# Kernel tuning notes

Measured on AMD Instinct MI355X. Metric: run time of the kernel, lower is better.

## Reference

```python
import jax, jax.numpy as jnp
import numpy as np

N, L, S, D, H = 4, 8192, 8192, 256, 8
DH = D // H  # 32
EPS_ATTN = 1e-6
EPS_LN = 1e-5


def setup_inputs() -> dict:
    key = jax.random.key(0)
    ks = jax.random.split(key, 8)
    w = lambda k, sh: jax.random.normal(k, sh, jnp.float32) * 0.02
    return {
        "x": jax.random.normal(ks[0], (N, L, D), jnp.float32),
        "source": jax.random.normal(ks[1], (N, S, D), jnp.float32),
        "Wq": w(ks[2], (D, D)),
        "Wk": w(ks[3], (D, D)),
        "Wv": w(ks[4], (D, D)),
        "Wm": w(ks[5], (D, D)),
        "W1": w(ks[6], (2 * D, 2 * D)),
        "W2": w(ks[7], (2 * D, D)),
        "g1": jnp.ones((D,), jnp.float32),
        "b1": jnp.zeros((D,), jnp.float32),
        "g2": jnp.ones((D,), jnp.float32),
        "b2": jnp.zeros((D,), jnp.float32),
    }


def _layernorm(x, g, b):
    m = jnp.mean(x, axis=-1, keepdims=True)
    v = jnp.var(x, axis=-1, keepdims=True)
    return (x - m) * jax.lax.rsqrt(v + EPS_LN) * g + b


def reference(x, source, Wq, Wk, Wv, Wm, W1, W2, g1, b1, g2, b2):
    bs = x.shape[0]
    # QKV projections (bias=False), split heads -> [N, L/S, H, DH]
    q = (x @ Wq).reshape(bs, -1, H, DH)
    k = (source @ Wk).reshape(bs, -1, H, DH)
    v = (source @ Wv).reshape(bs, -1, H, DH)
    # elu+1 feature map (linear attention, LoFTR-style)
    Q = jax.nn.elu(q) + 1.0
    K = jax.nn.elu(k) + 1.0
    v_len = v.shape[1]
    vals = v / v_len
    KV = jnp.einsum("nshd,nshv->nhdv", K, vals)  # [N, H, DH, DH]
    Z = 1.0 / (jnp.einsum("nlhd,nhd->nlh", Q, K.sum(axis=1)) + EPS_ATTN)
    msg = jnp.einsum("nlhd,nhdv,nlh->nlhv", Q, KV, Z) * v_len  # [N, L, H, DH]
    # merge heads + LN
    msg = msg.reshape(bs, -1, H * DH) @ Wm
    msg = _layernorm(msg, g1, b1)
    # concat-MLP with LeakyReLU(0.1)
    h = jnp.concatenate([x, msg], axis=2) @ W1
    h = jnp.where(h >= 0, h, 0.1 * h)
    msg = h @ W2
    msg = _layernorm(msg, g2, b2)
    return x + msg
```

## Files before the change

### kernel.cpp

```cpp
#include <hip/hip_runtime.h>

typedef __bf16 bf16;
typedef __bf16 bf16x4 __attribute__((ext_vector_type(4)));
typedef __bf16 bf16x8 __attribute__((ext_vector_type(8)));
typedef float f32x4 __attribute__((ext_vector_type(4)));

__device__ __forceinline__ float apply_epi(float v, int epi) {
  if (epi == 1) return v > 0.f ? v + 1.f : __expf(v);
  if (epi == 2) return v >= 0.f ? v : 0.1f * v;
  return v;
}

__device__ __forceinline__ void g2l16(const bf16* gp, bf16* lp) {
  __builtin_amdgcn_global_load_lds(
      (const __attribute__((address_space(1))) void*)gp,
      (__attribute__((address_space(3))) void*)lp, 16, 0, 0);
}

__global__ void detect_kernel(const unsigned* g1raw, int* flag) {
  if (threadIdx.x == 0 && blockIdx.x == 0)
    *flag = (g1raw[0] == 0x3F800000u) ? 1 : 0;
}

struct TransArgs {
  const void* src[6];
  bf16* dst[6];
  int R[6], C[6], t0[6];
};

__global__ __launch_bounds__(256) void prep_kernel(
    const void* __restrict__ xin, const void* __restrict__ sin,
    bf16* __restrict__ bx, bf16* __restrict__ bs,
    TransArgs ta, const int* flagp) {
  const bool f32 = (*flagp != 0);
  if (blockIdx.x < 8192) {
    const void* s;
    bf16* d;
    size_t i;
    if (blockIdx.x < 4096) {
      s = xin; d = bx; i = (size_t)blockIdx.x * 2048 + threadIdx.x * 8;
    } else {
      s = sin; d = bs; i = (size_t)(blockIdx.x - 4096) * 2048 + threadIdx.x * 8;
    }
    if (f32) {
      f32x4 lo = *(const f32x4*)((const float*)s + i);
      f32x4 hi = *(const f32x4*)((const float*)s + i + 4);
      bf16x8 t;
      t[0] = (bf16)lo[0]; t[1] = (bf16)lo[1]; t[2] = (bf16)lo[2]; t[3] = (bf16)lo[3];
      t[4] = (bf16)hi[0]; t[5] = (bf16)hi[1]; t[6] = (bf16)hi[2]; t[7] = (bf16)hi[3];
      *(bf16x8*)(d + i) = t;
    } else {
      *(bf16x8*)(d + i) = *(const bf16x8*)((const bf16*)s + i);
    }
    return;
  }
  __shared__ bf16 tile[32][33];
  int bid = blockIdx.x - 8192;
  int si = 0;
#pragma unroll
  for (int i = 1; i < 6; ++i)
    if (bid >= ta.t0[i]) si = i;
  const void* srcv = ta.src[si];
  bf16* dst = ta.dst[si];
  int R = ta.R[si], Cc = ta.C[si];
  int lt = bid - ta.t0[si];
  int tpr = Cc >> 5;
  int tr = lt / tpr, tc = lt % tpr;
  int tx = threadIdx.x & 31, ty0 = threadIdx.x >> 5;
#pragma unroll
  for (int i = 0; i < 4; ++i) {
    int ty = ty0 + i * 8;
    size_t idx = (size_t)(tr * 32 + ty) * Cc + tc * 32 + tx;
    tile[ty][tx] = f32 ? (bf16)((const float*)srcv)[idx] : ((const bf16*)srcv)[idx];
  }
  __syncthreads();
#pragma unroll
  for (int i = 0; i < 4; ++i) {
    int ty = ty0 + i * 8;
    dst[(size_t)(tc * 32 + ty) * R + tr * 32 + tx] = tile[tx][ty];
  }
}

#define TM 256
#define TN 256
#define TK 64

__device__ __forceinline__ void stage_tile(
    const bf16* __restrict__ Ab, int ldA, int m0, int kcol,
    const bf16* __restrict__ Bt, int Kk, int n0, int kk,
    bf16* As, bf16* Bs, int tid) {
#pragma unroll
  for (int it = 0; it < 4; ++it) {
    int id = it * 512 + tid;
    int rr = id >> 3, pp = id & 7, gg = pp ^ (rr & 7);
    g2l16(Ab + (size_t)(m0 + rr) * ldA + kcol + gg * 8, As + id * 8);
  }
#pragma unroll
  for (int it = 0; it < 4; ++it) {
    int id = it * 512 + tid;
    int rr = id >> 3, pp = id & 7, gg = pp ^ (rr & 7);
    g2l16(Bt + (size_t)(n0 + rr) * Kk + kk + gg * 8, Bs + id * 8);
  }
}

__global__ __launch_bounds__(512, 2) void gemm256(
    const bf16* __restrict__ A, const bf16* __restrict__ A2, int ldA,
    const bf16* __restrict__ Bt, bf16* __restrict__ C, int Nn, int Kk, int epi,
    bf16* __restrict__ C2, int epi2, int split, int gridM) {
  __shared__ bf16 As[2][TM * TK];
  __shared__ bf16 Bs[2][TN * TK];
  const int tid = threadIdx.x;

  const int nwg = gridDim.x;
  const int cpx = nwg >> 3;
  const int swz = (blockIdx.x & 7) * cpx + (blockIdx.x >> 3);
  const int mb = swz % gridM, nb = swz / gridM;
  const int m0 = mb * TM, n0 = nb * TN;

  const int wave = tid >> 6, lane = tid & 63;
  const int wm = (wave >> 2) * 128, wn = (wave & 3) * 64;
  const int q = lane >> 4, mr = lane & 15;

  f32x4 acc[8][4];
#pragma unroll
  for (int i = 0; i < 8; ++i)
#pragma unroll
    for (int j = 0; j < 4; ++j) acc[i][j] = (f32x4){0.f, 0.f, 0.f, 0.f};

  const int kTiles = Kk / TK;

  stage_tile(A, ldA, m0, 0, Bt, Kk, n0, 0, As[0], Bs[0], tid);

  for (int kt = 0; kt < kTiles; ++kt) {
    const int nxt = kt + 1;
    if (nxt < kTiles) {
      int kk = nxt * TK;
      const bf16* Ab = A;
      int kcol = kk;
      if (A2 && kk >= 256) { Ab = A2; kcol = kk - 256; }
      stage_tile(Ab, ldA, m0, kcol, Bt, Kk, n0, kk, As[nxt & 1], Bs[nxt & 1], tid);
      asm volatile("s_waitcnt vmcnt(8)\n\ts_barrier" ::: "memory");
    } else {
      asm volatile("s_waitcnt vmcnt(0)\n\ts_barrier" ::: "memory");
    }
    const bf16* Asb = As[kt & 1];
    const bf16* Bsb = Bs[kt & 1];
#pragma unroll
    for (int ks = 0; ks < 2; ++ks) {
      bf16x8 af[8], bfv[4];
#pragma unroll
      for (int mi = 0; mi < 8; ++mi) {
        int rrow = wm + mi * 16 + mr;
        af[mi] = *(const bf16x8*)&Asb[rrow * TK + ((ks * 4 + q) ^ (rrow & 7)) * 8];
      }
#pragma unroll
      for (int ni = 0; ni < 4; ++ni) {
        int rrow = wn + ni * 16 + mr;
        bfv[ni] = *(const bf16x8*)&Bsb[rrow * TK + ((ks * 4 + q) ^ (rrow & 7)) * 8];
      }
#pragma unroll
      for (int mi = 0; mi < 8; ++mi)
#pragma unroll
        for (int ni = 0; ni < 4; ++ni)
          acc[mi][ni] = __builtin_amdgcn_mfma_f32_16x16x32_bf16(af[mi], bfv[ni], acc[mi][ni], 0, 0, 0);
    }
    asm volatile("s_waitcnt lgkmcnt(0)\n\ts_barrier" ::: "memory");
  }

  bf16* Cw = C;
  int nbase = n0, ep = epi;
  if (C2 && n0 >= split) { Cw = C2; nbase = n0 - split; ep = epi2; }
#pragma unroll
  for (int mi = 0; mi < 8; ++mi)
#pragma unroll
    for (int ni = 0; ni < 4; ++ni)
#pragma unroll
      for (int r4 = 0; r4 < 4; ++r4) {
        int row = m0 + wm + mi * 16 + q * 4 + r4;
        int cn = nbase + wn + ni * 16 + mr;
        float v = apply_epi(acc[mi][ni][r4], ep);
        Cw[(size_t)row * Nn + cn] = (bf16)v;
      }
}

#define KVCH 256
__global__ __launch_bounds__(256) void kv_kernel(
    const bf16* __restrict__ Kf, const bf16* __restrict__ V,
    float* __restrict__ partial, float* __restrict__ pk) {
  __shared__ bf16 Ks[KVCH][32];
  __shared__ bf16 Vs[KVCH][32];
  const int cb = blockIdx.x, h = blockIdx.y, n = blockIdx.z;
  const int tid = threadIdx.x;
  const int wave = tid >> 6, lane = tid & 63;
  const int d0 = (lane & 7) * 4, dv0 = (lane >> 3) * 4;
  const int s0 = cb * KVCH;
#pragma unroll
  for (int rd = 0; rd < 4; ++rd) {
    int rr = rd * 64 + (tid >> 2), pp = tid & 3;
    size_t g = ((size_t)(n * 8192 + s0 + rr)) * 256 + h * 32 + pp * 8;
    *(bf16x8*)&Ks[rr][pp * 8] = *(const bf16x8*)(Kf + g);
    *(bf16x8*)&Vs[rr][pp * 8] = *(const bf16x8*)(V + g);
  }
  __syncthreads();
  float acc[4][4] = {};
  float ks4[4] = {};
#pragma unroll 4
  for (int si = 0; si < 64; ++si) {
    int s = wave * 64 + si;
    bf16x4 k4 = *(const bf16x4*)&Ks[s][d0];
    bf16x4 v4 = *(const bf16x4*)&Vs[s][dv0];
    float kf[4] = {(float)k4[0], (float)k4[1], (float)k4[2], (float)k4[3]};
    float vf[4] = {(float)v4[0], (float)v4[1], (float)v4[2], (float)v4[3]};
#pragma unroll
    for (int vi = 0; vi < 4; ++vi)
#pragma unroll
      for (int di = 0; di < 4; ++di) acc[vi][di] = fmaf(vf[vi], kf[di], acc[vi][di]);
#pragma unroll
    for (int di = 0; di < 4; ++di) ks4[di] += kf[di];
  }
  __syncthreads();
  float* red = (float*)&Ks[0][0];
  float* ksr = (float*)&Vs[0][0];
#pragma unroll
  for (int vi = 0; vi < 4; ++vi)
#pragma unroll
    for (int di = 0; di < 4; ++di)
      red[wave * 1024 + (dv0 + vi) * 32 + d0 + di] = acc[vi][di];
  if (dv0 == 0) {
#pragma unroll
    for (int di = 0; di < 4; ++di) ksr[wave * 32 + d0 + di] = ks4[di];
  }
  __syncthreads();
  const size_t slot = (size_t)(n * 8 + h) * 32 + cb;
  f32x4 s4 = {0.f, 0.f, 0.f, 0.f};
#pragma unroll
  for (int w = 0; w < 4; ++w) s4 += *(const f32x4*)&red[w * 1024 + tid * 4];
  *(f32x4*)&partial[slot * 1024 + tid * 4] = s4;
  if (tid < 32) {
    float ss = 0.f;
#pragma unroll
    for (int w = 0; w < 4; ++w) ss += ksr[w * 32 + tid];
    pk[slot * 32 + tid] = ss;
  }
}

__global__ __launch_bounds__(256) void kv_reduce(
    const float* __restrict__ partial, const float* __restrict__ pk,
    float* __restrict__ kv_acc, float* __restrict__ ksum) {
  const int b = blockIdx.x;
  const int t = threadIdx.x;
  f32x4 s4 = {0.f, 0.f, 0.f, 0.f};
  for (int c = 0; c < 32; ++c)
    s4 += *(const f32x4*)&partial[((size_t)b * 32 + c) * 1024 + t * 4];
  *(f32x4*)&kv_acc[(size_t)b * 1024 + t * 4] = s4;
  if (t < 32) {
    float ss = 0.f;
    for (int c = 0; c < 32; ++c) ss += pk[((size_t)b * 32 + c) * 32 + t];
    ksum[(size_t)b * 32 + t] = ss;
  }
}

__global__ __launch_bounds__(256) void msg_kernel(
    const bf16* __restrict__ Q, const float* __restrict__ kv_acc,
    const float* __restrict__ ksum, bf16* __restrict__ msg) {
  __shared__ bf16 kvt[8][32][32];
  __shared__ float ksl[8][32];
  __shared__ float zl[8][128];
  int tid = threadIdx.x;
  int row0 = blockIdx.x * 128;
  int n = row0 >> 13;
  const float* kvb = kv_acc + (size_t)n * 8192;
  for (int i = tid; i < 8192; i += 256) ((bf16*)kvt)[i] = (bf16)kvb[i];
  ((float*)ksl)[tid] = ksum[(size_t)n * 256 + tid];
  __syncthreads();
  int r = tid & 127, hg = tid >> 7;
  const bf16* qrow = Q + (size_t)(row0 + r) * 256;
#pragma unroll
  for (int hh = 0; hh < 4; ++hh) {
    int h = hg * 4 + hh;
    float dot = 0.f;
#pragma unroll
    for (int d = 0; d < 32; ++d) dot = fmaf((float)qrow[h * 32 + d], ksl[h][d], dot);
    zl[h][r] = 1.f / (dot + 1e-6f);
  }
  __syncthreads();
  int wave = tid >> 6, lane = tid & 63, q = lane >> 4, mr = lane & 15;
  f32x4 zero = {0.f, 0.f, 0.f, 0.f};
  for (int h = 0; h < 8; ++h) {
    bf16x8 b0 = *(const bf16x8*)&kvt[h][mr][q * 8];
    bf16x8 b1 = *(const bf16x8*)&kvt[h][16 + mr][q * 8];
#pragma unroll
    for (int mi = 0; mi < 2; ++mi) {
      int arow = wave * 32 + mi * 16 + mr;
      bf16x8 a = *(const bf16x8*)(Q + (size_t)(row0 + arow) * 256 + h * 32 + q * 8);
      f32x4 c0 = __builtin_amdgcn_mfma_f32_16x16x32_bf16(a, b0, zero, 0, 0, 0);
      f32x4 c1 = __builtin_amdgcn_mfma_f32_16x16x32_bf16(a, b1, zero, 0, 0, 0);
#pragma unroll
      for (int r4 = 0; r4 < 4; ++r4) {
        int orow = wave * 32 + mi * 16 + q * 4 + r4;
        float z = zl[h][orow];
        size_t ob = (size_t)(row0 + orow) * 256 + h * 32;
        msg[ob + mr] = (bf16)(c0[r4] * z);
        msg[ob + 16 + mr] = (bf16)(c1[r4] * z);
      }
    }
  }
}

__global__ __launch_bounds__(256) void ln_kernel(
    const bf16* __restrict__ in, const void* __restrict__ g, const void* __restrict__ b,
    const void* __restrict__ resid, void* __restrict__ outp,
    const int* flagp, int ioDual) {
  const bool gbF32 = (*flagp != 0);
  const bool ioF32 = ioDual && gbF32;
  int wave = threadIdx.x >> 6, lane = threadIdx.x & 63;
  size_t row = (size_t)blockIdx.x * 4 + wave;
  int c = lane * 4;
  bf16x4 v = *(const bf16x4*)(in + row * 256 + c);
  float x0 = (float)v[0], x1 = (float)v[1], x2 = (float)v[2], x3 = (float)v[3];
  float s = x0 + x1 + x2 + x3;
  float sq = x0 * x0 + x1 * x1 + x2 * x2 + x3 * x3;
#pragma unroll
  for (int o = 32; o > 0; o >>= 1) {
    s += __shfl_xor(s, o);
    sq += __shfl_xor(sq, o);
  }
  float mean = s * (1.f / 256.f);
  float var = sq * (1.f / 256.f) - mean * mean;
  float rstd = rsqrtf(var + 1e-5f);
  float g0, g1v, g2v, g3, b0, b1v, b2v, b3;
  if (gbF32) {
    f32x4 gv = *(const f32x4*)((const float*)g + c);
    f32x4 bv = *(const f32x4*)((const float*)b + c);
    g0 = gv[0]; g1v = gv[1]; g2v = gv[2]; g3 = gv[3];
    b0 = bv[0]; b1v = bv[1]; b2v = bv[2]; b3 = bv[3];
  } else {
    bf16x4 gv = *(const bf16x4*)((const bf16*)g + c);
    bf16x4 bv = *(const bf16x4*)((const bf16*)b + c);
    g0 = (float)gv[0]; g1v = (float)gv[1]; g2v = (float)gv[2]; g3 = (float)gv[3];
    b0 = (float)bv[0]; b1v = (float)bv[1]; b2v = (float)bv[2]; b3 = (float)bv[3];
  }
  float y0 = (x0 - mean) * rstd * g0 + b0;
  float y1 = (x1 - mean) * rstd * g1v + b1v;
  float y2 = (x2 - mean) * rstd * g2v + b2v;
  float y3 = (x3 - mean) * rstd * g3 + b3;
  if (resid) {
    if (ioF32) {
      f32x4 rv = *(const f32x4*)((const float*)resid + row * 256 + c);
      y0 += rv[0]; y1 += rv[1]; y2 += rv[2]; y3 += rv[3];
    } else {
      bf16x4 rv = *(const bf16x4*)((const bf16*)resid + row * 256 + c);
      y0 += (float)rv[0]; y1 += (float)rv[1]; y2 += (float)rv[2]; y3 += (float)rv[3];
    }
  }
  if (ioF32) {
    f32x4 o4 = {y0, y1, y2, y3};
    *(f32x4*)((float*)outp + row * 256 + c) = o4;
  } else {
    bf16x4 o4;
    o4[0] = (bf16)y0; o4[1] = (bf16)y1; o4[2] = (bf16)y2; o4[3] = (bf16)y3;
    *(bf16x4*)((bf16*)outp + row * 256 + c) = o4;
  }
}

extern "C" void kernel_launch(void* const* d_in, const int* in_sizes, int n_in,
                              void* d_out, int out_size, void* d_ws, size_t ws_size,
                              hipStream_t stream) {
  const void* x   = d_in[0];
  const void* src = d_in[1];
  const void* Wq  = d_in[2];
  const void* Wk  = d_in[3];
  const void* Wv  = d_in[4];
  const void* Wm  = d_in[5];
  const void* W1  = d_in[6];
  const void* W2  = d_in[7];
  const void* g1  = d_in[8];
  const void* b1  = d_in[9];
  const void* g2  = d_in[10];
  const void* b2  = d_in[11];

  char* ws = (char*)d_ws;
  bf16* bufA = (bf16*)(ws);
  bf16* bufB = (bf16*)(ws + ((size_t)16 << 20));
  bf16* bufC = (bf16*)(ws + ((size_t)32 << 20));
  bf16* WqT  = (bf16*)(ws + ((size_t)48 << 20));
  bf16* WkvT = WqT + 65536;
  bf16* WmT  = WkvT + 131072;
  bf16* W1T  = WmT + 65536;
  bf16* W2T  = W1T + 262144;
  float* kv_acc = (float*)(ws + ((size_t)50 << 20));
  float* ksum = kv_acc + 32768;
  int* flagp = (int*)(ws + ((size_t)50 << 20) + 160 * 1024);
  float* partial = (float*)(ws + ((size_t)51 << 20));
  float* pk = (float*)(ws + ((size_t)55 << 20));
  bf16* bufX = (bf16*)d_out;
  bf16* bufS = bufX + 8388608;

  detect_kernel<<<dim3(1), dim3(64), 0, stream>>>((const unsigned*)g1, flagp);

  TransArgs ta;
  ta.src[0] = Wq; ta.src[1] = Wk; ta.src[2] = Wv; ta.src[3] = Wm; ta.src[4] = W1; ta.src[5] = W2;
  ta.dst[0] = WqT; ta.dst[1] = WkvT; ta.dst[2] = WkvT + 65536; ta.dst[3] = WmT; ta.dst[4] = W1T; ta.dst[5] = W2T;
  ta.R[0] = 256; ta.R[1] = 256; ta.R[2] = 256; ta.R[3] = 256; ta.R[4] = 512; ta.R[5] = 512;
  ta.C[0] = 256; ta.C[1] = 256; ta.C[2] = 256; ta.C[3] = 256; ta.C[4] = 512; ta.C[5] = 256;
  ta.t0[0] = 0; ta.t0[1] = 64; ta.t0[2] = 128; ta.t0[3] = 192; ta.t0[4] = 256; ta.t0[5] = 512;
  prep_kernel<<<dim3(8832), dim3(256), 0, stream>>>(x, src, bufX, bufS, ta, flagp);

  gemm256<<<dim3(128), dim3(512), 0, stream>>>(bufX, nullptr, 256, WqT, bufA, 256, 256, 1,
                                               nullptr, 0, 0, 128);
  gemm256<<<dim3(256), dim3(512), 0, stream>>>(bufS, nullptr, 256, WkvT, bufB, 256, 256, 1,
                                               bufC, 0, 256, 128);

  kv_kernel<<<dim3(32, 8, 4), dim3(256), 0, stream>>>(bufB, bufC, partial, pk);
  kv_reduce<<<dim3(32), dim3(256), 0, stream>>>(partial, pk, kv_acc, ksum);

  msg_kernel<<<dim3(256), dim3(256), 0, stream>>>(bufA, kv_acc, ksum, bufB);

  gemm256<<<dim3(128), dim3(512), 0, stream>>>(bufB, nullptr, 256, WmT, bufA, 256, 256, 0,
                                               nullptr, 0, 0, 128);

  ln_kernel<<<dim3(8192), dim3(256), 0, stream>>>(bufA, g1, b1, nullptr, bufC, flagp, 0);

  gemm256<<<dim3(256), dim3(512), 0, stream>>>(bufX, bufC, 256, W1T, bufA, 512, 512, 2,
                                               nullptr, 0, 0, 128);

  gemm256<<<dim3(128), dim3(512), 0, stream>>>(bufA, nullptr, 512, W2T, bufC, 256, 512, 0,
                                               nullptr, 0, 0, 128);

  ln_kernel<<<dim3(8192), dim3(256), 0, stream>>>(bufC, g2, b2, x, d_out, flagp, 1);
}
```

Before: 293.4 us.

## Restructure gemm256 main loop into phased half-tile staging interleaved with MFMA

The GEMM K-loop is rebuilt so that each 64-wide K tile is split into A and B halves of 128 rows. Global-to-LDS loads for upcoming halves are issued between sub-blocks of MFMA work, with fine-grained barriers and vmcnt waits, and s_setprio is raised around the MFMA clusters. The goal is to overlap memory staging with matrix math and to raise MFMA issue priority over other waves. The cost is many more barriers per tile and a more intricate schedule that assumes an even number of K tiles.

```diff
diff --git a/kernel.cpp b/kernel.cpp
--- a/kernel.cpp
+++ b/kernel.cpp
@@ -85,30 +85,11 @@
 #define TN 256
 #define TK 64
 
-__device__ __forceinline__ void stage_tile(
-    const bf16* __restrict__ Ab, int ldA, int m0, int kcol,
-    const bf16* __restrict__ Bt, int Kk, int n0, int kk,
-    bf16* As, bf16* Bs, int tid) {
-#pragma unroll
-  for (int it = 0; it < 4; ++it) {
-    int id = it * 512 + tid;
-    int rr = id >> 3, pp = id & 7, gg = pp ^ (rr & 7);
-    g2l16(Ab + (size_t)(m0 + rr) * ldA + kcol + gg * 8, As + id * 8);
-  }
-#pragma unroll
-  for (int it = 0; it < 4; ++it) {
-    int id = it * 512 + tid;
-    int rr = id >> 3, pp = id & 7, gg = pp ^ (rr & 7);
-    g2l16(Bt + (size_t)(n0 + rr) * Kk + kk + gg * 8, Bs + id * 8);
-  }
-}
-
 __global__ __launch_bounds__(512, 2) void gemm256(
     const bf16* __restrict__ A, const bf16* __restrict__ A2, int ldA,
     const bf16* __restrict__ Bt, bf16* __restrict__ C, int Nn, int Kk, int epi,
     bf16* __restrict__ C2, int epi2, int split, int gridM) {
-  __shared__ bf16 As[2][TM * TK];
-  __shared__ bf16 Bs[2][TN * TK];
+  __shared__ bf16 lds[2][2][2][128 * 64];
   const int tid = threadIdx.x;
 
   const int nwg = gridDim.x;
@@ -120,6 +101,10 @@
   const int wave = tid >> 6, lane = tid & 63;
   const int wm = (wave >> 2) * 128, wn = (wave & 3) * 64;
   const int q = lane >> 4, mr = lane & 15;
+  const int ahalf = wm >> 7, bhalf = wn >> 7;
+  const int bro = wn & 64;
+
+  const int kTiles = Kk / TK;
 
   f32x4 acc[8][4];
 #pragma unroll
@@ -127,45 +112,137 @@
 #pragma unroll
     for (int j = 0; j < 4; ++j) acc[i][j] = (f32x4){0.f, 0.f, 0.f, 0.f};
 
-  const int kTiles = Kk / TK;
-
-  stage_tile(A, ldA, m0, 0, Bt, Kk, n0, 0, As[0], Bs[0], tid);
-
-  for (int kt = 0; kt < kTiles; ++kt) {
-    const int nxt = kt + 1;
-    if (nxt < kTiles) {
-      int kk = nxt * TK;
-      const bf16* Ab = A;
-      int kcol = kk;
-      if (A2 && kk >= 256) { Ab = A2; kcol = kk - 256; }
-      stage_tile(Ab, ldA, m0, kcol, Bt, Kk, n0, kk, As[nxt & 1], Bs[nxt & 1], tid);
-      asm volatile("s_waitcnt vmcnt(8)\n\ts_barrier" ::: "memory");
-    } else {
-      asm volatile("s_waitcnt vmcnt(0)\n\ts_barrier" ::: "memory");
-    }
-    const bf16* Asb = As[kt & 1];
-    const bf16* Bsb = Bs[kt & 1];
-#pragma unroll
-    for (int ks = 0; ks < 2; ++ks) {
-      bf16x8 af[8], bfv[4];
-#pragma unroll
-      for (int mi = 0; mi < 8; ++mi) {
-        int rrow = wm + mi * 16 + mr;
-        af[mi] = *(const bf16x8*)&Asb[rrow * TK + ((ks * 4 + q) ^ (rrow & 7)) * 8];
-      }
-#pragma unroll
-      for (int ni = 0; ni < 4; ++ni) {
-        int rrow = wn + ni * 16 + mr;
-        bfv[ni] = *(const bf16x8*)&Bsb[rrow * TK + ((ks * 4 + q) ^ (rrow & 7)) * 8];
-      }
-#pragma unroll
-      for (int mi = 0; mi < 8; ++mi)
-#pragma unroll
-        for (int ni = 0; ni < 4; ++ni)
-          acc[mi][ni] = __builtin_amdgcn_mfma_f32_16x16x32_bf16(af[mi], bfv[ni], acc[mi][ni], 0, 0, 0);
-    }
-    asm volatile("s_waitcnt lgkmcnt(0)\n\ts_barrier" ::: "memory");
-  }
+  auto stageA = [&](int t, int half) {
+    const bf16* Ab = A;
+    int kcol = t * TK;
+    if (A2 && kcol >= 256) { Ab = A2; kcol -= 256; }
+    bf16* dst = &lds[t & 1][0][half][0];
+#pragma unroll
+    for (int ld = 0; ld < 2; ++ld) {
+      int id = ld * 512 + tid;
+      int rr = id >> 3, pp = id & 7, gg = pp ^ (rr & 7);
+      g2l16(Ab + (size_t)(m0 + half * 128 + rr) * ldA + kcol + gg * 8, dst + id * 8);
+    }
+  };
+  auto stageB = [&](int t, int half) {
+    bf16* dst = &lds[t & 1][1][half][0];
+    int kk = t * TK;
+#pragma unroll
+    for (int ld = 0; ld < 2; ++ld) {
+      int id = ld * 512 + tid;
+      int rr = id >> 3, pp = id & 7, gg = pp ^ (rr & 7);
+      g2l16(Bt + (size_t)(n0 + half * 128 + rr) * Kk + kk + gg * 8, dst + id * 8);
+    }
+  };
+
+  bf16x8 af[8], bfr[8];
+  auto rdA = [&](const bf16* base, int mlo) {
+#pragma unroll
+    for (int i = 0; i < 4; ++i) {
+      int r = (mlo + i) * 16 + mr;
+#pragma unroll
+      for (int ks = 0; ks < 2; ++ks)
+        af[i * 2 + ks] = *(const bf16x8*)&base[r * TK + (((ks * 4 + q) ^ (r & 7)) * 8)];
+    }
+  };
+  auto rdB = [&](bf16x8* bo, const bf16* base, int nlo) {
+#pragma unroll
+    for (int i = 0; i < 2; ++i) {
+      int r = bro + (nlo + i) * 16 + mr;
+#pragma unroll
+      for (int ks = 0; ks < 2; ++ks)
+        bo[i * 2 + ks] = *(const bf16x8*)&base[r * TK + (((ks * 4 + q) ^ (r & 7)) * 8)];
+    }
+  };
+  auto mma = [&](const bf16x8* bo, int mlo, int nlo) {
+    __builtin_amdgcn_s_setprio(1);
+#pragma unroll
+    for (int i = 0; i < 4; ++i)
+#pragma unroll
+      for (int j = 0; j < 2; ++j)
+#pragma unroll
+        for (int ks = 0; ks < 2; ++ks)
+          acc[mlo + i][nlo + j] = __builtin_amdgcn_mfma_f32_16x16x32_bf16(
+              af[i * 2 + ks], bo[j * 2 + ks], acc[mlo + i][nlo + j], 0, 0, 0);
+    __builtin_amdgcn_s_setprio(0);
+  };
+
+#define PH_END asm volatile("s_waitcnt lgkmcnt(0)\n\ts_barrier" ::: "memory")
+#define PH_END_VM asm volatile("s_waitcnt vmcnt(4) lgkmcnt(0)\n\ts_barrier" ::: "memory")
+#define PH_END_VM0 asm volatile("s_waitcnt vmcnt(0) lgkmcnt(0)\n\ts_barrier" ::: "memory")
+
+  stageB(0, 0); stageB(0, 1); stageA(0, 0); stageA(0, 1); stageB(1, 0); stageB(1, 1);
+  asm volatile("s_waitcnt vmcnt(4)\n\ts_barrier" ::: "memory");
+
+  const bf16* A0 = &lds[0][0][ahalf][0];
+  const bf16* B0 = &lds[0][1][bhalf][0];
+  const bf16* A1 = &lds[1][0][ahalf][0];
+  const bf16* B1 = &lds[1][1][bhalf][0];
+
+  const int nIter = kTiles >> 1;
+  for (int p = 0; p < nIter - 1; ++p) {
+    const int t0 = 2 * p, t1 = 2 * p + 1;
+    rdA(A0, 0); rdB(bfr + 0, B0, 0);
+    stageA(t1, 0);
+    mma(bfr + 0, 0, 0);
+    PH_END;
+    rdB(bfr + 4, B0, 2);
+    stageA(t1, 1);
+    mma(bfr + 4, 0, 2);
+    PH_END;
+    rdA(A0, 4);
+    stageB(t0 + 2, 0);
+    mma(bfr + 0, 4, 0);
+    PH_END;
+    stageB(t0 + 2, 1);
+    mma(bfr + 4, 4, 2);
+    PH_END_VM;
+    rdA(A1, 0); rdB(bfr + 0, B1, 0);
+    stageA(t0 + 2, 0);
+    mma(bfr + 0, 0, 0);
+    PH_END;
+    rdB(bfr + 4, B1, 2);
+    stageA(t0 + 2, 1);
+    mma(bfr + 4, 0, 2);
+    PH_END;
+    rdA(A1, 4);
+    stageB(t1 + 2, 0);
+    mma(bfr + 0, 4, 0);
+    PH_END;
+    stageB(t1 + 2, 1);
+    mma(bfr + 4, 4, 2);
+    PH_END_VM;
+  }
+  {
+    const int t1 = kTiles - 1;
+    rdA(A0, 0); rdB(bfr + 0, B0, 0);
+    stageA(t1, 0);
+    mma(bfr + 0, 0, 0);
+    PH_END;
+    rdB(bfr + 4, B0, 2);
+    stageA(t1, 1);
+    mma(bfr + 4, 0, 2);
+    PH_END;
+    rdA(A0, 4);
+    mma(bfr + 0, 4, 0);
+    PH_END;
+    mma(bfr + 4, 4, 2);
+    PH_END_VM0;
+    rdA(A1, 0); rdB(bfr + 0, B1, 0);
+    mma(bfr + 0, 0, 0);
+    PH_END;
+    rdB(bfr + 4, B1, 2);
+    mma(bfr + 4, 0, 2);
+    PH_END;
+    rdA(A1, 4);
+    mma(bfr + 0, 4, 0);
+    PH_END;
+    mma(bfr + 4, 4, 2);
+    asm volatile("s_waitcnt lgkmcnt(0)" ::: "memory");
+  }
+#undef PH_END
+#undef PH_END_VM
+#undef PH_END_VM0
 
   bf16* Cw = C;
   int nbase = n0, ep = epi;
```

Result: no change. 292.6 us (-0.3%).
